# Optimization experiments

Measured on AMD Instinct MI355X. Metric: run time of the kernel, lower is better.

The kernel has to match this reference:

```python
import jax, jax.numpy as jnp
import numpy as np

NEG_SLOPE = 0.2
BN_EPS = 1e-5
SM_EPS = 1e-16


def gatv2_conv(x, src, dst, num_nodes, Wl, bl, Wr, br, att, bias, concat):
    # x: [N, Fin]; att: [H, C]
    H, C = att.shape
    xl = (x @ Wl + bl).reshape(-1, H, C)  # source-side (x_j), lin_l
    xr = (x @ Wr + br).reshape(-1, H, C)  # target-side (x_i), lin_r
    e = jax.nn.leaky_relu(xl[src] + xr[dst], NEG_SLOPE)          # [E, H, C]
    logits = jnp.einsum('ehc,hc->eh', e, att)                    # [E, H]
    m = jax.ops.segment_max(logits, dst, num_segments=num_nodes)  # [N, H]
    expv = jnp.exp(logits - m[dst])
    denom = jax.ops.segment_sum(expv, dst, num_segments=num_nodes)
    alpha = expv / (denom[dst] + SM_EPS)                          # [E, H]
    msg = xl[src] * alpha[:, :, None]                             # [E, H, C]
    out = jax.ops.segment_sum(msg, dst, num_segments=num_nodes)   # [N, H, C]
    out = out.reshape(num_nodes, H * C) if concat else out.mean(axis=1)
    return out + bias


def batchnorm(x, gamma, beta):
    mean = x.mean(axis=0)
    var = x.var(axis=0)  # biased, as torch uses for normalization
    return gamma * (x - mean) * jax.lax.rsqrt(var + BN_EPS) + beta


def setup_inputs() -> dict:
    key = jax.random.key(0)
    ks = jax.random.split(key, 16)
    N, E = 50000, 800000
    Fin, Hid, Out, H = 128, 64, 64, 4
    s = 0.05
    inp = {
        'x': jax.random.normal(ks[0], (N, Fin), jnp.float32),
        'edge_index': jax.random.randint(ks[1], (2, E), 0, N, jnp.int64),
        # conv1 (heads=4, concat=False)
        'Wl1': jax.random.normal(ks[2], (Fin, H * Hid), jnp.float32) * s,
        'bl1': jnp.zeros((H * Hid,), jnp.float32),
        'Wr1': jax.random.normal(ks[3], (Fin, H * Hid), jnp.float32) * s,
        'br1': jnp.zeros((H * Hid,), jnp.float32),
        'att1': jax.random.normal(ks[4], (H, Hid), jnp.float32) * s,
        'bias1': jnp.zeros((Hid,), jnp.float32),
        'g1': jnp.ones((Hid,), jnp.float32),
        'beta1': jnp.zeros((Hid,), jnp.float32),
        # conv2 (heads=1, concat=True -> same as single head)
        'Wl2': jax.random.normal(ks[5], (Hid, Out), jnp.float32) * s,
        'bl2': jnp.zeros((Out,), jnp.float32),
        'Wr2': jax.random.normal(ks[6], (Hid, Out), jnp.float32) * s,
        'br2': jnp.zeros((Out,), jnp.float32),
        'att2': jax.random.normal(ks[7], (1, Out), jnp.float32) * s,
        'bias2': jnp.zeros((Out,), jnp.float32),
        'g2': jnp.ones((Out,), jnp.float32),
        'beta2': jnp.zeros((Out,), jnp.float32),
    }
    return inp


def reference(x, edge_index, Wl1, bl1, Wr1, br1, att1, bias1, g1, beta1,
              Wl2, bl2, Wr2, br2, att2, bias2, g2, beta2):
    N = x.shape[0]
    loops = jnp.arange(N, dtype=edge_index.dtype)  # PyG add_self_loops=True
    src = jnp.concatenate([edge_index[0], loops])
    dst = jnp.concatenate([edge_index[1], loops])
    h = gatv2_conv(x, src, dst, N, Wl1, bl1, Wr1, br1, att1, bias1, concat=False)
    h = jax.nn.relu(batchnorm(h, g1, beta1))  # dropout = identity (eval)
    h = gatv2_conv(h, src, dst, N, Wl2, bl2, Wr2, br2, att2, bias2, concat=True)
    h = jax.nn.relu(batchnorm(h, g2, beta2))
    return h
```

## Files before the change

### kernel.cpp

```cpp
#include <hip/hip_runtime.h>
#include <hip/hip_bf16.h>
#include <math.h>

#define TPB 256

typedef __attribute__((ext_vector_type(8))) _Float16 hfrag8;
typedef __attribute__((ext_vector_type(2))) _Float16 h2;
typedef __attribute__((ext_vector_type(4))) float f32x4;

union HU { unsigned int u; h2 h; };

static __device__ __forceinline__ h2 as_h2(unsigned int u) { HU c; c.u = u; return c.h; }
static __device__ __forceinline__ unsigned short f2h_bits(float f) {
  union { _Float16 h; unsigned short s; } c; c.h = (_Float16)f; return c.s;
}

#define DPP_ROR(v, C) __int_as_float(__builtin_amdgcn_update_dpp( \
    __float_as_int(v), __float_as_int(v), (C), 0xf, 0xf, false))
static __device__ __forceinline__ float red16(float p) {
  p += DPP_ROR(p, 0x121);
  p += DPP_ROR(p, 0x122);
  p += DPP_ROR(p, 0x124);
  p += DPP_ROR(p, 0x128);
  return p;
}

__global__ void k_deg_wprep(const int* __restrict__ ei, int E, int ET, int* __restrict__ deg,
                            const float* __restrict__ Wl1, const float* __restrict__ Wr1,
                            const float* __restrict__ Wl2, const float* __restrict__ Wr2,
                            unsigned short* __restrict__ wt1l, unsigned short* __restrict__ wt1r,
                            unsigned short* __restrict__ wt2l, unsigned short* __restrict__ wt2r,
                            int egrid) {
  int b = blockIdx.x;
  if (b < egrid) {
    int e = b * TPB + threadIdx.x;
    if (e < ET) {
      int dst = (e < E) ? ei[E + e] : (e - E);
      atomicAdd(&deg[dst], 1);
    }
    return;
  }
  int i = (b - egrid) * TPB + threadIdx.x;
  if (i < 32768) {
    int c = i >> 7, k = i & 127;
    wt1l[i] = f2h_bits(Wl1[(size_t)k * 256 + c]);
  } else if (i < 65536) {
    int j = i - 32768; int c = j >> 7, k = j & 127;
    wt1r[j] = f2h_bits(Wr1[(size_t)k * 256 + c]);
  } else if (i < 69632) {
    int j = i - 65536; int c = j >> 6, k = j & 63;
    wt2l[j] = f2h_bits(Wl2[(size_t)k * 64 + c]);
  } else if (i < 73728) {
    int j = i - 69632; int c = j >> 6, k = j & 63;
    wt2r[j] = f2h_bits(Wr2[(size_t)k * 64 + c]);
  }
}

__global__ void k_scanf(const int* __restrict__ deg, int N,
                        int* __restrict__ rowoff, int* __restrict__ cursor) {
  __shared__ int sm[TPB];
  int t = threadIdx.x;
  int pref = blockIdx.x * TPB;
  int acc = 0;
  for (int j = t; j < pref; j += TPB) acc += (deg[j] + 3) & ~3;
  sm[t] = acc;
  __syncthreads();
  for (int d = TPB / 2; d > 0; d >>= 1) {
    if (t < d) sm[t] += sm[t + d];
    __syncthreads();
  }
  int base = sm[0];
  __syncthreads();
  int i = pref + t;
  int v = (i < N) ? ((deg[i] + 3) & ~3) : 0;
  sm[t] = v;
  __syncthreads();
  for (int d = 1; d < TPB; d <<= 1) {
    int tmp = (t >= d) ? sm[t - d] : 0;
    __syncthreads();
    sm[t] += tmp;
    __syncthreads();
  }
  if (i < N) {
    int off = base + sm[t] - v;
    rowoff[i] = off;
    cursor[i] = off;
  }
}

__global__ void k_fill(const int* __restrict__ ei, int E, int ET,
                       int* __restrict__ cursor, int* __restrict__ csrc) {
  int e = blockIdx.x * blockDim.x + threadIdx.x;
  if (e >= ET) return;
  int src, dst;
  if (e < E) { src = ei[e]; dst = ei[E + e]; } else { src = dst = e - E; }
  int pos = atomicAdd(&cursor[dst], 1);
  csrc[pos] = src;
}

__global__ void k_gemm_mfma(const float* __restrict__ A, const float* __restrict__ affine,
                            const unsigned short* __restrict__ Wt0, const float* __restrict__ b0,
                            const unsigned short* __restrict__ Wt1, const float* __restrict__ b1,
                            unsigned short* __restrict__ out0, unsigned short* __restrict__ out1,
                            int M, int K, int Nc) {
  extern __shared__ short lds[];
  short* As = lds;
  short* Bls = lds + 64 * K;
  short* Brs = lds + 128 * K;
  const int r0 = blockIdx.x * 64, n0 = blockIdx.y * 64;
  const int tid = threadIdx.x;
  const int Kb = K * 2;

  const int fpr = K >> 2;
  for (int idx = tid; idx < 64 * fpr; idx += TPB) {
    int row = idx / fpr, c4 = idx - row * fpr;
    int gr = r0 + row;
    float4 v = make_float4(0.f, 0.f, 0.f, 0.f);
    if (gr < M) v = *(const float4*)(A + (size_t)gr * K + c4 * 4);
    if (affine) {
      int c = c4 * 4;
      v.x = fmaxf(v.x * affine[c + 0] + affine[64 + c + 0], 0.f);
      v.y = fmaxf(v.y * affine[c + 1] + affine[64 + c + 1], 0.f);
      v.z = fmaxf(v.z * affine[c + 2] + affine[64 + c + 2], 0.f);
      v.w = fmaxf(v.w * affine[c + 3] + affine[64 + c + 3], 0.f);
    }
    ushort4 pk;
    pk.x = f2h_bits(v.x); pk.y = f2h_bits(v.y); pk.z = f2h_bits(v.z); pk.w = f2h_bits(v.w);
    int kb = (c4 * 8) ^ ((row & 7) << 4);
    *(ushort4*)((char*)As + row * Kb + kb) = pk;
  }
  const int cpr = K >> 3;
  for (int idx = tid; idx < 64 * cpr; idx += TPB) {
    int c = idx / cpr, k8 = (idx - c * cpr) * 8;
    int kb = (k8 * 2) ^ ((c & 7) << 4);
    uint4 w0 = *(const uint4*)(Wt0 + (size_t)(n0 + c) * K + k8);
    *(uint4*)((char*)Bls + c * Kb + kb) = w0;
    uint4 w1 = *(const uint4*)(Wt1 + (size_t)(n0 + c) * K + k8);
    *(uint4*)((char*)Brs + c * Kb + kb) = w1;
  }
  __syncthreads();

  const int w = tid >> 6, lane = tid & 63;
  const int arow = w * 16 + (lane & 15);
  const int l16 = (lane >> 4) << 3;
  f32x4 accL[4], accR[4];
#pragma unroll
  for (int i = 0; i < 4; ++i) { accL[i] = (f32x4)0.f; accR[i] = (f32x4)0.f; }
  for (int k0 = 0; k0 < K; k0 += 32) {
    int kb = (k0 + l16) * 2;
    hfrag8 af = *(hfrag8*)((char*)As + arow * Kb + (kb ^ ((arow & 7) << 4)));
#pragma unroll
    for (int cf = 0; cf < 4; ++cf) {
      int col = cf * 16 + (lane & 15);
      int cb = col * Kb + (kb ^ ((col & 7) << 4));
      hfrag8 bl = *(hfrag8*)((char*)Bls + cb);
      accL[cf] = __builtin_amdgcn_mfma_f32_16x16x32_f16(af, bl, accL[cf], 0, 0, 0);
      hfrag8 br = *(hfrag8*)((char*)Brs + cb);
      accR[cf] = __builtin_amdgcn_mfma_f32_16x16x32_f16(af, br, accR[cf], 0, 0, 0);
    }
  }
  const int rbase = r0 + w * 16 + ((lane >> 4) << 2);
  const int cbase = n0 + (lane & 15);
#pragma unroll
  for (int cf = 0; cf < 4; ++cf) {
    int gcol = cbase + cf * 16;
    float bb0 = b0[gcol], bb1 = b1[gcol];
#pragma unroll
    for (int r = 0; r < 4; ++r) {
      int grow = rbase + r;
      if (grow < M) {
        out0[(size_t)grow * Nc + gcol] = f2h_bits(accL[cf][r] + bb0);
        out1[(size_t)grow * Nc + gcol] = f2h_bits(accR[cf][r] + bb1);
      }
    }
  }
}

__global__ __launch_bounds__(TPB) void k_gat1(
    const unsigned short* __restrict__ xl, const unsigned short* __restrict__ xr,
    const int* __restrict__ rowoff, const int* __restrict__ deg,
    const int* __restrict__ csrc,
    const float* __restrict__ att, const float* __restrict__ bias,
    float* __restrict__ out, int N) {
  int node = (blockIdx.x * TPB + threadIdx.x) >> 6;
  int lane = threadIdx.x & 63;
  if (node >= N) return;
  int l4 = lane * 4;
  float4 atv = *(const float4*)(att + l4);
  h2 at01, at23;
  at01.x = (_Float16)atv.x; at01.y = (_Float16)atv.y;
  at23.x = (_Float16)atv.z; at23.y = (_Float16)atv.w;
  float4 bb = *(const float4*)(bias + l4);
  uint2 rv = *(const uint2*)(xr + (node << 8) + l4);
  h2 xr01 = as_h2(rv.x), xr23 = as_h2(rv.y);
  const _Float16 c02 = (_Float16)0.2f;
  int beg = rowoff[node];
  int dg = deg[node];
  int endR = beg + dg;
  int endF = beg + (dg & ~3);
  float s = 0.f, a0 = 0.f, a1 = 0.f, a2 = 0.f, a3 = 0.f;
  int k = beg;
  for (; k < endF; k += 4) {
    int4 q = *(const int4*)(csrc + k);
    uint2 vv[4];
    vv[0] = *(const uint2*)(xl + (q.x << 8) + l4);
    vv[1] = *(const uint2*)(xl + (q.y << 8) + l4);
    vv[2] = *(const uint2*)(xl + (q.z << 8) + l4);
    vv[3] = *(const uint2*)(xl + (q.w << 8) + l4);
    float ps[4];
#pragma unroll
    for (int u = 0; u < 4; ++u) {
      h2 x01 = as_h2(vv[u].x), x23 = as_h2(vv[u].y);
      h2 t01 = x01 + xr01, t23 = x23 + xr23;
      h2 l01 = __builtin_elementwise_max(t01, t01 * c02);
      h2 l23 = __builtin_elementwise_max(t23, t23 * c02);
      ps[u] = __builtin_amdgcn_fdot2(l01, at01,
              __builtin_amdgcn_fdot2(l23, at23, 0.f, false), false);
    }
#pragma unroll
    for (int u = 0; u < 4; ++u) ps[u] = red16(ps[u]);
#pragma unroll
    for (int u = 0; u < 4; ++u) {
      float wv = __expf(ps[u]);
      h2 x01 = as_h2(vv[u].x), x23 = as_h2(vv[u].y);
      s += wv;
      a0 += wv * (float)x01.x; a1 += wv * (float)x01.y;
      a2 += wv * (float)x23.x; a3 += wv * (float)x23.y;
    }
  }
  if (k < endR) {
    int4 q = *(const int4*)(csrc + k);
    uint2 vv[4];
    vv[0] = *(const uint2*)(xl + (q.x << 8) + l4);
    vv[1] = *(const uint2*)(xl + (q.y << 8) + l4);
    vv[2] = *(const uint2*)(xl + (q.z << 8) + l4);
    vv[3] = *(const uint2*)(xl + (q.w << 8) + l4);
    float ps[4];
#pragma unroll
    for (int u = 0; u < 4; ++u) {
      h2 x01 = as_h2(vv[u].x), x23 = as_h2(vv[u].y);
      h2 t01 = x01 + xr01, t23 = x23 + xr23;
      h2 l01 = __builtin_elementwise_max(t01, t01 * c02);
      h2 l23 = __builtin_elementwise_max(t23, t23 * c02);
      ps[u] = __builtin_amdgcn_fdot2(l01, at01,
              __builtin_amdgcn_fdot2(l23, at23, 0.f, false), false);
    }
#pragma unroll
    for (int u = 0; u < 4; ++u) ps[u] = red16(ps[u]);
#pragma unroll
    for (int u = 0; u < 4; ++u) {
      float wv = (k + u < endR) ? __expf(ps[u]) : 0.f;
      h2 x01 = as_h2(vv[u].x), x23 = as_h2(vv[u].y);
      s += wv;
      a0 += wv * (float)x01.x; a1 += wv * (float)x01.y;
      a2 += wv * (float)x23.x; a3 += wv * (float)x23.y;
    }
  }
  float inv = 1.f / (s + 1e-16f);
  a0 *= inv; a1 *= inv; a2 *= inv; a3 *= inv;
  a0 += __shfl_xor(a0, 16); a0 += __shfl_xor(a0, 32);
  a1 += __shfl_xor(a1, 16); a1 += __shfl_xor(a1, 32);
  a2 += __shfl_xor(a2, 16); a2 += __shfl_xor(a2, 32);
  a3 += __shfl_xor(a3, 16); a3 += __shfl_xor(a3, 32);
  if (lane < 16) {
    float4 o;
    o.x = a0 * 0.25f + bb.x;
    o.y = a1 * 0.25f + bb.y;
    o.z = a2 * 0.25f + bb.z;
    o.w = a3 * 0.25f + bb.w;
    *(float4*)(out + (node << 6) + l4) = o;
  }
}

__global__ __launch_bounds__(TPB) void k_gat2(
    const unsigned short* __restrict__ xl, const unsigned short* __restrict__ xr,
    const int* __restrict__ rowoff, const int* __restrict__ deg,
    const int* __restrict__ csrc,
    const float* __restrict__ att, const float* __restrict__ bias,
    float* __restrict__ out, int N) {
  int node = (blockIdx.x * TPB + threadIdx.x) >> 6;
  int lane = threadIdx.x & 63;
  if (node >= N) return;
  int grp = lane >> 4, c4 = (lane & 15) * 4;
  float4 atv = *(const float4*)(att + c4);
  h2 at01, at23;
  at01.x = (_Float16)atv.x; at01.y = (_Float16)atv.y;
  at23.x = (_Float16)atv.z; at23.y = (_Float16)atv.w;
  float4 bb = *(const float4*)(bias + c4);
  uint2 rv = *(const uint2*)(xr + (node << 6) + c4);
  h2 xr01 = as_h2(rv.x), xr23 = as_h2(rv.y);
  const _Float16 c02 = (_Float16)0.2f;
  int beg = rowoff[node];
  int dg = deg[node];
  int endR = beg + dg;
  int quads = (dg + 3) >> 2;
  float s = 0.f, a0 = 0.f, a1 = 0.f, a2 = 0.f, a3 = 0.f;
  for (int it = 0; it < quads; ++it) {
    int kk = beg + it * 4 + grp;
    int src = csrc[kk];
    bool ok = kk < endR;
    uint2 v = *(const uint2*)(xl + (src << 6) + c4);
    h2 x01 = as_h2(v.x), x23 = as_h2(v.y);
    h2 t01 = x01 + xr01, t23 = x23 + xr23;
    h2 l01 = __builtin_elementwise_max(t01, t01 * c02);
    h2 l23 = __builtin_elementwise_max(t23, t23 * c02);
    float p = __builtin_amdgcn_fdot2(l01, at01,
              __builtin_amdgcn_fdot2(l23, at23, 0.f, false), false);
    p = red16(p);
    float wv = ok ? __expf(p) : 0.f;
    s += wv;
    a0 += wv * (float)x01.x; a1 += wv * (float)x01.y;
    a2 += wv * (float)x23.x; a3 += wv * (float)x23.y;
  }
  s += __shfl_xor(s, 16); s += __shfl_xor(s, 32);
  a0 += __shfl_xor(a0, 16); a0 += __shfl_xor(a0, 32);
  a1 += __shfl_xor(a1, 16); a1 += __shfl_xor(a1, 32);
  a2 += __shfl_xor(a2, 16); a2 += __shfl_xor(a2, 32);
  a3 += __shfl_xor(a3, 16); a3 += __shfl_xor(a3, 32);
  if (lane < 16) {
    float inv = 1.f / (s + 1e-16f);
    float4 o;
    o.x = a0 * inv + bb.x;
    o.y = a1 * inv + bb.y;
    o.z = a2 * inv + bb.z;
    o.w = a3 * inv + bb.w;
    *(float4*)(out + (node << 6) + c4) = o;
  }
}

__global__ void k_bnstatfin(const float* __restrict__ in, int N, float* __restrict__ part,
                            int* __restrict__ counter, const float* __restrict__ g,
                            const float* __restrict__ beta, float* __restrict__ ab) {
  __shared__ float sm[TPB], sq[TPB];
  __shared__ float fin[TPB];
  __shared__ int lastsm;
  int col = threadIdx.x & 63;
  int rq = threadIdx.x >> 6;
  float s0 = 0.f, q0 = 0.f, s1 = 0.f, q1 = 0.f;
  int stride = gridDim.x * 4;
  int r = blockIdx.x * 4 + rq;
  for (; r + stride < N; r += 2 * stride) {
    float v0 = in[(size_t)r * 64 + col];
    float v1 = in[(size_t)(r + stride) * 64 + col];
    s0 += v0; q0 += v0 * v0;
    s1 += v1; q1 += v1 * v1;
  }
  if (r < N) {
    float v0 = in[(size_t)r * 64 + col];
    s0 += v0; q0 += v0 * v0;
  }
  sm[threadIdx.x] = s0 + s1; sq[threadIdx.x] = q0 + q1;
  __syncthreads();
  if (threadIdx.x < 128) {
    float v;
    if (threadIdx.x < 64) {
      v = sm[threadIdx.x] + sm[threadIdx.x + 64] + sm[threadIdx.x + 128] + sm[threadIdx.x + 192];
    } else {
      int c = threadIdx.x - 64;
      v = sq[c] + sq[c + 64] + sq[c + 128] + sq[c + 192];
    }
    part[(size_t)blockIdx.x * 128 + threadIdx.x] = v;
  }
  __threadfence();
  __syncthreads();
  if (threadIdx.x == 0) lastsm = atomicAdd(counter, 1);
  __syncthreads();
  if (lastsm != gridDim.x - 1) return;
  __threadfence();
  int t = threadIdx.x;
  int c = t & 127, gidx = t >> 7;
  int B = gridDim.x;
  float acc0 = 0.f, acc1 = 0.f, acc2 = 0.f, acc3 = 0.f;
  int b = gidx;
  for (; b + 6 < B; b += 8) {
    acc0 += part[(size_t)b * 128 + c];
    acc1 += part[(size_t)(b + 2) * 128 + c];
    acc2 += part[(size_t)(b + 4) * 128 + c];
    acc3 += part[(size_t)(b + 6) * 128 + c];
  }
  for (; b < B; b += 2) acc0 += part[(size_t)b * 128 + c];
  fin[t] = (acc0 + acc1) + (acc2 + acc3);
  __syncthreads();
  if (t < 64) {
    float ts = fin[t] + fin[t + 128];
    float tq = fin[t + 64] + fin[t + 192];
    float mean = ts / (float)N;
    float var = tq / (float)N - mean * mean;
    float a = g[t] * rsqrtf(var + 1e-5f);
    ab[t] = a;
    ab[64 + t] = beta[t] - mean * a;
  }
}

__global__ void k_bnapply(const float* __restrict__ in, const float* __restrict__ ab,
                          float* __restrict__ out, int total4) {
  int idx = blockIdx.x * blockDim.x + threadIdx.x;
  if (idx >= total4) return;
  float4 v = *(const float4*)(in + (size_t)idx * 4);
  int c0 = (idx & 15) * 4;
  v.x = fmaxf(v.x * ab[c0 + 0] + ab[64 + c0 + 0], 0.f);
  v.y = fmaxf(v.y * ab[c0 + 1] + ab[64 + c0 + 1], 0.f);
  v.z = fmaxf(v.z * ab[c0 + 2] + ab[64 + c0 + 2], 0.f);
  v.w = fmaxf(v.w * ab[c0 + 3] + ab[64 + c0 + 3], 0.f);
  *(float4*)(out + (size_t)idx * 4) = v;
}

extern "C" void kernel_launch(void* const* d_in, const int* in_sizes, int n_in,
                              void* d_out, int out_size, void* d_ws, size_t ws_size,
                              hipStream_t stream) {
  const float* x     = (const float*)d_in[0];
  const int*   ei    = (const int*)d_in[1];
  const float* Wl1   = (const float*)d_in[2];
  const float* bl1   = (const float*)d_in[3];
  const float* Wr1   = (const float*)d_in[4];
  const float* br1   = (const float*)d_in[5];
  const float* att1  = (const float*)d_in[6];
  const float* bias1 = (const float*)d_in[7];
  const float* g1    = (const float*)d_in[8];
  const float* be1   = (const float*)d_in[9];
  const float* Wl2   = (const float*)d_in[10];
  const float* bl2   = (const float*)d_in[11];
  const float* Wr2   = (const float*)d_in[12];
  const float* br2   = (const float*)d_in[13];
  const float* att2  = (const float*)d_in[14];
  const float* bias2 = (const float*)d_in[15];
  const float* g2    = (const float*)d_in[16];
  const float* be2   = (const float*)d_in[17];
  float* out = (float*)d_out;

  const int N  = in_sizes[0] / 128;
  const int E  = in_sizes[1] / 2;
  const int ET = E + N;
  const int ETP = ET + 4 * ((N + 255) & ~255);
  const int SB = (N + TPB - 1) / TPB;

  char* p = (char*)d_ws;
  auto take = [&](size_t b) { char* q = p; p += (b + 255) & ~(size_t)255; return q; };

  unsigned short* xl1 = (unsigned short*)take((size_t)N * 256 * 2);
  unsigned short* xr1 = (unsigned short*)take((size_t)N * 256 * 2);
  unsigned short* xl2 = (unsigned short*)take((size_t)N * 64 * 2);
  unsigned short* xr2 = (unsigned short*)take((size_t)N * 64 * 2);
  float* out1 = (float*)take((size_t)N * 64 * 4);
  unsigned short* wt1l = (unsigned short*)take(256 * 128 * 2);
  unsigned short* wt1r = (unsigned short*)take(256 * 128 * 2);
  unsigned short* wt2l = (unsigned short*)take(64 * 64 * 2);
  unsigned short* wt2r = (unsigned short*)take(64 * 64 * 2);
  int* deg    = (int*)take((size_t)N * 4);
  int* ctr    = (int*)take(512);
  int* csrc   = (int*)take((size_t)ETP * 4 + 16);
  size_t zero_bytes = (char*)(csrc + ETP) + 16 - (char*)deg;
  int* rowoff = (int*)take((size_t)(N + 1) * 4);
  int* cursor = (int*)take((size_t)N * 4);
  float* part = (float*)take((size_t)256 * 128 * 4);
  float* ab1  = (float*)take(128 * 4);
  float* ab2  = (float*)take(128 * 4);
  (void)ws_size; (void)n_in; (void)out_size;

  int egrid = (ET + TPB - 1) / TPB;
  int wgrid = (73728 + TPB - 1) / TPB;
  int ngrid = (N + 3) / 4;
  int mtile = (N + 63) / 64;
  int total4 = N * 16;

  hipMemsetAsync(deg, 0, zero_bytes, stream);
  k_deg_wprep<<<egrid + wgrid, TPB, 0, stream>>>(ei, E, ET, deg, Wl1, Wr1, Wl2, Wr2,
                                                 wt1l, wt1r, wt2l, wt2r, egrid);
  k_scanf<<<SB, TPB, 0, stream>>>(deg, N, rowoff, cursor);
  k_fill<<<egrid, TPB, 0, stream>>>(ei, E, ET, cursor, csrc);

  k_gemm_mfma<<<dim3(mtile, 4), TPB, 3 * 64 * 128 * 2, stream>>>(
      x, nullptr, wt1l, bl1, wt1r, br1, xl1, xr1, N, 128, 256);
  k_gat1<<<ngrid, TPB, 0, stream>>>(xl1, xr1, rowoff, deg, csrc, att1, bias1, out1, N);
  k_bnstatfin<<<256, TPB, 0, stream>>>(out1, N, part, ctr, g1, be1, ab1);

  k_gemm_mfma<<<dim3(mtile, 1), TPB, 3 * 64 * 64 * 2, stream>>>(
      out1, ab1, wt2l, bl2, wt2r, br2, xl2, xr2, N, 64, 64);
  k_gat2<<<ngrid, TPB, 0, stream>>>(xl2, xr2, rowoff, deg, csrc, att2, bias2, out, N);
  k_bnstatfin<<<256, TPB, 0, stream>>>(out, N, part, ctr + 64, g2, be2, ab2);
  k_bnapply<<<(total4 + TPB - 1) / TPB, TPB, 0, stream>>>(out, ab2, out, total4);
}
```

Baseline: 364.5 us.

## Fuse CSR build and final BatchNorm into cooperative kernels with grid sync

Replaces the memset plus degree, scan and fill kernels with one cooperative kernel that separates its phases with grid-wide syncs and uses a two-level block-sum scan. It also merges the second BatchNorm stats and apply steps into one cooperative kernel, and remaps the first GEMM's blocks so that each group of 8 consecutive block IDs covers 8 row tiles (one per XCD) for the same column tile. The aim is to remove several launch gaps and the memset. In exchange, the grid is limited to co-resident blocks, the scan and tail fill run serially per block (thread 0 writes every row offset), and csrc padding is zeroed explicitly.

```diff
diff --git a/kernel.cpp b/kernel.cpp
--- a/kernel.cpp
+++ b/kernel.cpp
@@ -1,6 +1,9 @@
 #include <hip/hip_runtime.h>
 #include <hip/hip_bf16.h>
+#include <hip/hip_cooperative_groups.h>
 #include <math.h>
+
+namespace cg = cooperative_groups;
 
 #define TPB 256
 
@@ -25,89 +28,111 @@
   return p;
 }
 
-__global__ void k_deg_wprep(const int* __restrict__ ei, int E, int ET, int* __restrict__ deg,
-                            const float* __restrict__ Wl1, const float* __restrict__ Wr1,
-                            const float* __restrict__ Wl2, const float* __restrict__ Wr2,
-                            unsigned short* __restrict__ wt1l, unsigned short* __restrict__ wt1r,
-                            unsigned short* __restrict__ wt2l, unsigned short* __restrict__ wt2r,
-                            int egrid) {
-  int b = blockIdx.x;
-  if (b < egrid) {
-    int e = b * TPB + threadIdx.x;
-    if (e < ET) {
-      int dst = (e < E) ? ei[E + e] : (e - E);
-      atomicAdd(&deg[dst], 1);
-    }
-    return;
-  }
-  int i = (b - egrid) * TPB + threadIdx.x;
-  if (i < 32768) {
-    int c = i >> 7, k = i & 127;
-    wt1l[i] = f2h_bits(Wl1[(size_t)k * 256 + c]);
-  } else if (i < 65536) {
-    int j = i - 32768; int c = j >> 7, k = j & 127;
-    wt1r[j] = f2h_bits(Wr1[(size_t)k * 256 + c]);
-  } else if (i < 69632) {
-    int j = i - 65536; int c = j >> 6, k = j & 63;
-    wt2l[j] = f2h_bits(Wl2[(size_t)k * 64 + c]);
-  } else if (i < 73728) {
-    int j = i - 69632; int c = j >> 6, k = j & 63;
-    wt2r[j] = f2h_bits(Wr2[(size_t)k * 64 + c]);
-  }
-}
-
-__global__ void k_scanf(const int* __restrict__ deg, int N,
-                        int* __restrict__ rowoff, int* __restrict__ cursor) {
+__global__ void k_csr(const int* __restrict__ ei, int E, int ET, int N,
+                      const float* __restrict__ Wl1, const float* __restrict__ Wr1,
+                      const float* __restrict__ Wl2, const float* __restrict__ Wr2,
+                      unsigned short* __restrict__ wt1l, unsigned short* __restrict__ wt1r,
+                      unsigned short* __restrict__ wt2l, unsigned short* __restrict__ wt2r,
+                      int* __restrict__ deg, int* __restrict__ ctr, int* __restrict__ bsum,
+                      int* __restrict__ rowoff, int* __restrict__ cursor,
+                      int* __restrict__ csrc) {
+  cg::grid_group grid = cg::this_grid();
   __shared__ int sm[TPB];
-  int t = threadIdx.x;
-  int pref = blockIdx.x * TPB;
+  const int gsz = gridDim.x * TPB;
+  const int tid = blockIdx.x * TPB + threadIdx.x;
+
+  for (int i = tid; i < N; i += gsz) deg[i] = 0;
+  if (tid < 128) ctr[tid] = 0;
+  __threadfence();
+  grid.sync();
+
+  for (int e = tid; e < ET; e += gsz) {
+    int dst = (e < E) ? ei[E + e] : (e - E);
+    atomicAdd(&deg[dst], 1);
+  }
+  for (int i = tid; i < 73728; i += gsz) {
+    if (i < 32768) {
+      int c = i >> 7, k = i & 127;
+      wt1l[i] = f2h_bits(Wl1[(size_t)k * 256 + c]);
+    } else if (i < 65536) {
+      int j = i - 32768; int c = j >> 7, k = j & 127;
+      wt1r[j] = f2h_bits(Wr1[(size_t)k * 256 + c]);
+    } else if (i < 69632) {
+      int j = i - 65536; int c = j >> 6, k = j & 63;
+      wt2l[j] = f2h_bits(Wl2[(size_t)k * 64 + c]);
+    } else {
+      int j = i - 69632; int c = j >> 6, k = j & 63;
+      wt2r[j] = f2h_bits(Wr2[(size_t)k * 64 + c]);
+    }
+  }
+  __threadfence();
+  grid.sync();
+
+  const int CHUNK = (N + gridDim.x - 1) / gridDim.x;
+  const int n0 = blockIdx.x * CHUNK;
+  const int n1 = min(n0 + CHUNK, N);
+  int a = 0;
+  for (int i = n0 + threadIdx.x; i < n1; i += TPB) a += (deg[i] + 3) & ~3;
+  sm[threadIdx.x] = a;
+  __syncthreads();
+  for (int d = TPB / 2; d > 0; d >>= 1) {
+    if (threadIdx.x < d) sm[threadIdx.x] += sm[threadIdx.x + d];
+    __syncthreads();
+  }
+  if (threadIdx.x == 0) bsum[blockIdx.x] = sm[0];
+  __threadfence();
+  grid.sync();
+
   int acc = 0;
-  for (int j = t; j < pref; j += TPB) acc += (deg[j] + 3) & ~3;
-  sm[t] = acc;
+  for (int j = threadIdx.x; j < blockIdx.x; j += TPB) acc += bsum[j];
+  __syncthreads();
+  sm[threadIdx.x] = acc;
   __syncthreads();
   for (int d = TPB / 2; d > 0; d >>= 1) {
-    if (t < d) sm[t] += sm[t + d];
+    if (threadIdx.x < d) sm[threadIdx.x] += sm[threadIdx.x + d];
     __syncthreads();
   }
-  int base = sm[0];
-  __syncthreads();
-  int i = pref + t;
-  int v = (i < N) ? ((deg[i] + 3) & ~3) : 0;
-  sm[t] = v;
-  __syncthreads();
-  for (int d = 1; d < TPB; d <<= 1) {
-    int tmp = (t >= d) ? sm[t - d] : 0;
-    __syncthreads();
-    sm[t] += tmp;
-    __syncthreads();
-  }
-  if (i < N) {
-    int off = base + sm[t] - v;
-    rowoff[i] = off;
-    cursor[i] = off;
-  }
-}
-
-__global__ void k_fill(const int* __restrict__ ei, int E, int ET,
-                       int* __restrict__ cursor, int* __restrict__ csrc) {
-  int e = blockIdx.x * blockDim.x + threadIdx.x;
-  if (e >= ET) return;
-  int src, dst;
-  if (e < E) { src = ei[e]; dst = ei[E + e]; } else { src = dst = e - E; }
-  int pos = atomicAdd(&cursor[dst], 1);
-  csrc[pos] = src;
+  if (threadIdx.x == 0) {
+    int run = sm[0];
+    for (int i = n0; i < n1; ++i) {
+      rowoff[i] = run;
+      cursor[i] = run;
+      run += (deg[i] + 3) & ~3;
+    }
+  }
+  __threadfence();
+  grid.sync();
+
+  for (int e = tid; e < ET; e += gsz) {
+    int src, dst;
+    if (e < E) { src = ei[e]; dst = ei[E + e]; } else { src = dst = e - E; }
+    csrc[atomicAdd(&cursor[dst], 1)] = src;
+  }
+  for (int i = tid; i < N; i += gsz) {
+    int beg = rowoff[i], dg = deg[i];
+    int pe = beg + ((dg + 3) & ~3);
+    for (int k = beg + dg; k < pe; ++k) csrc[k] = 0;
+  }
 }
 
 __global__ void k_gemm_mfma(const float* __restrict__ A, const float* __restrict__ affine,
                             const unsigned short* __restrict__ Wt0, const float* __restrict__ b0,
                             const unsigned short* __restrict__ Wt1, const float* __restrict__ b1,
                             unsigned short* __restrict__ out0, unsigned short* __restrict__ out1,
-                            int M, int K, int Nc) {
+                            int M, int K, int Nc, int mtile, int nt4) {
   extern __shared__ short lds[];
   short* As = lds;
   short* Bls = lds + 64 * K;
   short* Brs = lds + 128 * K;
-  const int r0 = blockIdx.x * 64, n0 = blockIdx.y * 64;
+  int m, nt;
+  if (nt4) {
+    int xcd = blockIdx.x & 7, gg = blockIdx.x >> 3;
+    nt = gg & 3; m = ((gg >> 2) << 3) | xcd;
+    if (m >= mtile) return;
+  } else {
+    m = blockIdx.x; nt = 0;
+  }
+  const int r0 = m * 64, n0 = nt * 64;
   const int tid = threadIdx.x;
   const int Kb = K * 2;
 
@@ -392,17 +417,85 @@
   }
 }
 
-__global__ void k_bnapply(const float* __restrict__ in, const float* __restrict__ ab,
-                          float* __restrict__ out, int total4) {
-  int idx = blockIdx.x * blockDim.x + threadIdx.x;
-  if (idx >= total4) return;
-  float4 v = *(const float4*)(in + (size_t)idx * 4);
-  int c0 = (idx & 15) * 4;
-  v.x = fmaxf(v.x * ab[c0 + 0] + ab[64 + c0 + 0], 0.f);
-  v.y = fmaxf(v.y * ab[c0 + 1] + ab[64 + c0 + 1], 0.f);
-  v.z = fmaxf(v.z * ab[c0 + 2] + ab[64 + c0 + 2], 0.f);
-  v.w = fmaxf(v.w * ab[c0 + 3] + ab[64 + c0 + 3], 0.f);
-  *(float4*)(out + (size_t)idx * 4) = v;
+__global__ void k_bn2(float* __restrict__ inout, int N, float* __restrict__ part,
+                      const float* __restrict__ g, const float* __restrict__ beta,
+                      float* __restrict__ ab, int total4) {
+  cg::grid_group grid = cg::this_grid();
+  __shared__ float sm[TPB], sq[TPB];
+  __shared__ float fin[TPB];
+  int col = threadIdx.x & 63;
+  int rq = threadIdx.x >> 6;
+  float s0 = 0.f, q0 = 0.f, s1 = 0.f, q1 = 0.f;
+  int stride = gridDim.x * 4;
+  int r = blockIdx.x * 4 + rq;
+  for (; r + stride < N; r += 2 * stride) {
+    float v0 = inout[(size_t)r * 64 + col];
+    float v1 = inout[(size_t)(r + stride) * 64 + col];
+    s0 += v0; q0 += v0 * v0;
+    s1 += v1; q1 += v1 * v1;
+  }
+  if (r < N) {
+    float v0 = inout[(size_t)r * 64 + col];
+    s0 += v0; q0 += v0 * v0;
+  }
+  sm[threadIdx.x] = s0 + s1; sq[threadIdx.x] = q0 + q1;
+  __syncthreads();
+  if (threadIdx.x < 128) {
+    float v;
+    if (threadIdx.x < 64) {
+      v = sm[threadIdx.x] + sm[threadIdx.x + 64] + sm[threadIdx.x + 128] + sm[threadIdx.x + 192];
+    } else {
+      int c = threadIdx.x - 64;
+      v = sq[c] + sq[c + 64] + sq[c + 128] + sq[c + 192];
+    }
+    part[(size_t)blockIdx.x * 128 + threadIdx.x] = v;
+  }
+  __threadfence();
+  grid.sync();
+  if (blockIdx.x == 0) {
+    int t = threadIdx.x;
+    int c = t & 127, gidx = t >> 7;
+    int B = gridDim.x;
+    float acc0 = 0.f, acc1 = 0.f, acc2 = 0.f, acc3 = 0.f;
+    int b = gidx;
+    for (; b + 6 < B; b += 8) {
+      acc0 += part[(size_t)b * 128 + c];
+      acc1 += part[(size_t)(b + 2) * 128 + c];
+      acc2 += part[(size_t)(b + 4) * 128 + c];
+      acc3 += part[(size_t)(b + 6) * 128 + c];
+    }
+    for (; b < B; b += 2) acc0 += part[(size_t)b * 128 + c];
+    fin[t] = (acc0 + acc1) + (acc2 + acc3);
+    __syncthreads();
+    if (t < 64) {
+      float ts = fin[t] + fin[t + 128];
+      float tq = fin[t + 64] + fin[t + 192];
+      float mean = ts / (float)N;
+      float var = tq / (float)N - mean * mean;
+      float a = g[t] * rsqrtf(var + 1e-5f);
+      ab[t] = a;
+      ab[64 + t] = beta[t] - mean * a;
+    }
+    __threadfence();
+  }
+  grid.sync();
+  __threadfence();
+  float a_c, b_c;
+  {
+    int c0 = (threadIdx.x & 15) * 4;
+    (void)c0;
+  }
+  int gsz = gridDim.x * TPB;
+  for (int idx = blockIdx.x * TPB + threadIdx.x; idx < total4; idx += gsz) {
+    float4 v = *(const float4*)(inout + (size_t)idx * 4);
+    int c0 = (idx & 15) * 4;
+    v.x = fmaxf(v.x * ab[c0 + 0] + ab[64 + c0 + 0], 0.f);
+    v.y = fmaxf(v.y * ab[c0 + 1] + ab[64 + c0 + 1], 0.f);
+    v.z = fmaxf(v.z * ab[c0 + 2] + ab[64 + c0 + 2], 0.f);
+    v.w = fmaxf(v.w * ab[c0 + 3] + ab[64 + c0 + 3], 0.f);
+    *(float4*)(inout + (size_t)idx * 4) = v;
+  }
+  (void)a_c; (void)b_c;
 }
 
 extern "C" void kernel_launch(void* const* d_in, const int* in_sizes, int n_in,
@@ -428,11 +521,10 @@
   const float* be2   = (const float*)d_in[17];
   float* out = (float*)d_out;
 
-  const int N  = in_sizes[0] / 128;
-  const int E  = in_sizes[1] / 2;
-  const int ET = E + N;
+  int N  = in_sizes[0] / 128;
+  int E  = in_sizes[1] / 2;
+  int ET = E + N;
   const int ETP = ET + 4 * ((N + 255) & ~255);
-  const int SB = (N + TPB - 1) / TPB;
 
   char* p = (char*)d_ws;
   auto take = [&](size_t b) { char* q = p; p += (b + 255) & ~(size_t)255; return q; };
@@ -449,34 +541,39 @@
   int* deg    = (int*)take((size_t)N * 4);
   int* ctr    = (int*)take(512);
   int* csrc   = (int*)take((size_t)ETP * 4 + 16);
-  size_t zero_bytes = (char*)(csrc + ETP) + 16 - (char*)deg;
   int* rowoff = (int*)take((size_t)(N + 1) * 4);
   int* cursor = (int*)take((size_t)N * 4);
+  int* bsum   = (int*)take((size_t)1024 * 4);
   float* part = (float*)take((size_t)256 * 128 * 4);
   float* ab1  = (float*)take(128 * 4);
   float* ab2  = (float*)take(128 * 4);
   (void)ws_size; (void)n_in; (void)out_size;
 
-  int egrid = (ET + TPB - 1) / TPB;
-  int wgrid = (73728 + TPB - 1) / TPB;
   int ngrid = (N + 3) / 4;
   int mtile = (N + 63) / 64;
+  int mg8 = (mtile + 7) / 8;
   int total4 = N * 16;
 
-  hipMemsetAsync(deg, 0, zero_bytes, stream);
-  k_deg_wprep<<<egrid + wgrid, TPB, 0, stream>>>(ei, E, ET, deg, Wl1, Wr1, Wl2, Wr2,
-                                                 wt1l, wt1r, wt2l, wt2r, egrid);
-  k_scanf<<<SB, TPB, 0, stream>>>(deg, N, rowoff, cursor);
-  k_fill<<<egrid, TPB, 0, stream>>>(ei, E, ET, cursor, csrc);
-
-  k_gemm_mfma<<<dim3(mtile, 4), TPB, 3 * 64 * 128 * 2, stream>>>(
-      x, nullptr, wt1l, bl1, wt1r, br1, xl1, xr1, N, 128, 256);
+  {
+    void* args[] = {(void*)&ei, (void*)&E, (void*)&ET, (void*)&N,
+                    (void*)&Wl1, (void*)&Wr1, (void*)&Wl2, (void*)&Wr2,
+                    (void*)&wt1l, (void*)&wt1r, (void*)&wt2l, (void*)&wt2r,
+                    (void*)&deg, (void*)&ctr, (void*)&bsum,
+                    (void*)&rowoff, (void*)&cursor, (void*)&csrc};
+    hipLaunchCooperativeKernel((void*)k_csr, dim3(1024), dim3(TPB), args, 0, stream);
+  }
+
+  k_gemm_mfma<<<mg8 * 32, TPB, 3 * 64 * 128 * 2, stream>>>(
+      x, nullptr, wt1l, bl1, wt1r, br1, xl1, xr1, N, 128, 256, mtile, 1);
   k_gat1<<<ngrid, TPB, 0, stream>>>(xl1, xr1, rowoff, deg, csrc, att1, bias1, out1, N);
   k_bnstatfin<<<256, TPB, 0, stream>>>(out1, N, part, ctr, g1, be1, ab1);
 
-  k_gemm_mfma<<<dim3(mtile, 1), TPB, 3 * 64 * 64 * 2, stream>>>(
-      out1, ab1, wt2l, bl2, wt2r, br2, xl2, xr2, N, 64, 64);
+  k_gemm_mfma<<<mtile, TPB, 3 * 64 * 64 * 2, stream>>>(
+      out1, ab1, wt2l, bl2, wt2r, br2, xl2, xr2, N, 64, 64, mtile, 0);
   k_gat2<<<ngrid, TPB, 0, stream>>>(xl2, xr2, rowoff, deg, csrc, att2, bias2, out, N);
-  k_bnstatfin<<<256, TPB, 0, stream>>>(out, N, part, ctr + 64, g2, be2, ab2);
-  k_bnapply<<<(total4 + TPB - 1) / TPB, TPB, 0, stream>>>(out, ab2, out, total4);
-}
+  {
+    void* args[] = {(void*)&out, (void*)&N, (void*)&part,
+                    (void*)&g2, (void*)&be2, (void*)&ab2, (void*)&total4};
+    hipLaunchCooperativeKernel((void*)k_bn2, dim3(256), dim3(TPB), args, 0, stream);
+  }
+}
```

Measured after the change: 1.048 ms. +187.5%, slower.
